# Performance work log

Measured on AMD Instinct MI355X. Metric: run time of the kernel, lower is better.

Reference implementation:

```python
import jax, jax.numpy as jnp
import numpy as np

IN_FEATURES = 16384
OUT_FEATURES = 16384
NNZ = 1_000_000
BATCH = 256


def setup_inputs() -> dict:
    key = jax.random.key(0)
    k_x, k_w, k_b, k_r, k_c = jax.random.split(key, 5)
    x = jax.random.normal(k_x, (BATCH, IN_FEATURES), dtype=jnp.float32)
    weight_vals = jax.random.normal(k_w, (NNZ,), dtype=jnp.float32)
    bias = jax.random.normal(k_b, (OUT_FEATURES,), dtype=jnp.float32)
    rows = jax.random.randint(k_r, (NNZ,), 0, OUT_FEATURES, dtype=jnp.int32)
    cols = jax.random.randint(k_c, (NNZ,), 0, IN_FEATURES, dtype=jnp.int32)
    return {"x": x, "weight_vals": weight_vals, "bias": bias,
            "rows": rows, "cols": cols}


def reference(x, weight_vals, bias, rows, cols):
    # SparseLinear forward: y = x @ W^T + b, with W sparse COO of shape
    # [out_features, in_features]; (rows, cols) are W's nnz coordinates.
    # Per-edge contribution: x[:, col] * W[row, col], scattered into out[:, row].
    contrib = x[:, cols] * weight_vals  # [B, nnz]
    # segment-sum edges into output features: [nnz, B] -> [out, B]
    out = jax.ops.segment_sum(contrib.T, rows, num_segments=OUT_FEATURES).T
    return out + bias  # [B, out_features]
```

## Files before the change

kernel.cpp:

```cpp
#include <hip/hip_runtime.h>
#include <hip/hip_bf16.h>
#include <hip/hip_fp16.h>

#define IN_F    16384
#define OUT_F   16384
#define CAP     128
#define NBUCK   512
#define CAPB    2560
#define EPB     2048
#define TBLK    1024

typedef unsigned int u32x4 __attribute__((ext_vector_type(4)));
typedef float f32x4 __attribute__((ext_vector_type(4)));
typedef float f32x2 __attribute__((ext_vector_type(2)));


__global__ void prep_kernel(const float* __restrict__ x,
                            __hip_bfloat16* __restrict__ xTh,
                            const int* __restrict__ rows,
                            const int* __restrict__ cols,
                            const float* __restrict__ vals, int nnz, int npart,
                            int* __restrict__ gcursor,
                            uint2* __restrict__ staging) {
    __shared__ __align__(16) union {
        float tile[64 * 65];
        struct {
            uint2 recs[EPB];
            int hist[NBUCK];
            int lstart[NBUCK];
            int gbase[NBUCK];
            int wsum[4];
            int total;
        } pa;
    } sm;
    int t = threadIdx.x;
    if ((int)blockIdx.x < npart) {
        sm.pa.hist[t] = 0; sm.pa.hist[t + 256] = 0;
        __syncthreads();
        int i0 = blockIdx.x * EPB;
        unsigned int pk[8], vb[8];
#pragma unroll
        for (int k = 0; k < 8; ++k) {
            int i = i0 + k * 256 + t;
            if (i < nnz) {
                int r = rows[i], c = cols[i];
                pk[k] = ((unsigned int)r << 14) | (unsigned int)c;
                vb[k] = ((unsigned int)c << 16) |
                        (unsigned int)__half_as_ushort(__float2half(vals[i]));
                atomicAdd(&sm.pa.hist[r >> 5], 1);
            } else pk[k] = 0xffffffffu;
        }
        __syncthreads();
        int lane = t & 63, w = t >> 6;
        int h0 = sm.pa.hist[2 * t], h1 = sm.pa.hist[2 * t + 1];
        int pv = h0 + h1;
        int incl = pv;
#pragma unroll
        for (int off = 1; off < 64; off <<= 1) {
            int u = __shfl_up(incl, off, 64);
            if (lane >= off) incl += u;
        }
        if (lane == 63) sm.pa.wsum[w] = incl;
        __syncthreads();
        int addw = 0;
#pragma unroll
        for (int q = 0; q < 3; ++q) addw += (q < w) ? sm.pa.wsum[q] : 0;
        incl += addw;
        int excl = incl - pv;
        sm.pa.lstart[2 * t]     = excl;
        sm.pa.lstart[2 * t + 1] = excl + h0;
        sm.pa.gbase[2 * t]     = h0 > 0 ? atomicAdd(&gcursor[2 * t], h0) : 0;
        sm.pa.gbase[2 * t + 1] = h1 > 0 ? atomicAdd(&gcursor[2 * t + 1], h1) : 0;
        if (t == 255) sm.pa.total = incl;
        sm.pa.hist[t] = 0; sm.pa.hist[t + 256] = 0;
        __syncthreads();
#pragma unroll
        for (int k = 0; k < 8; ++k) {
            if (pk[k] != 0xffffffffu) {
                int b = pk[k] >> 19;
                int pos = sm.pa.lstart[b] + atomicAdd(&sm.pa.hist[b], 1);
                sm.pa.recs[pos] = make_uint2(pk[k], vb[k]);
            }
        }
        __syncthreads();
        int total = sm.pa.total;
        for (int j = t; j < total; j += 256) {
            uint2 rec = sm.pa.recs[j];
            int b = rec.x >> 19;
            int gp = sm.pa.gbase[b] + (j - sm.pa.lstart[b]);
            if (gp < CAPB) {
                unsigned long long pvv =
                    (unsigned long long)rec.x | ((unsigned long long)rec.y << 32);
                __builtin_nontemporal_store(pvv,
                    (unsigned long long*)(staging + (size_t)b * CAPB + gp));
            }
        }
    } else {
        float* tile = (float*)&sm;
        int bid = blockIdx.x - npart;
        int i0 = (bid & 255) * 64;
        int b0 = (bid >> 8) * 64;
        int tx4 = t & 15;
        int r16 = t >> 4;
#pragma unroll
        for (int k = 0; k < 4; ++k) {
            int row = r16 + k * 16;
            f32x4 v = *(const f32x4*)(x + (size_t)(b0 + row) * IN_F + i0 + tx4 * 4);
            tile[row * 65 + tx4 * 4 + 0] = v.x;
            tile[row * 65 + tx4 * 4 + 1] = v.y;
            tile[row * 65 + tx4 * 4 + 2] = v.z;
            tile[row * 65 + tx4 * 4 + 3] = v.w;
        }
        __syncthreads();
        int tx = t & 63, ty = t >> 6;
        int h = b0 >> 7, j0 = b0 & 127;
#pragma unroll
        for (int k = 0; k < 64; k += 4) {
            int col = i0 + ty + k;
            xTh[((size_t)h * IN_F + col) * 128 + j0 + tx] =
                __float2bfloat16(tile[tx * 65 + ty + k]);
        }
    }
}


__global__ void __launch_bounds__(512, 4)
accum_kernel(const unsigned int* __restrict__ xh0,
             const uint2* __restrict__ staging,
             const int* __restrict__ gcursor,
             const float* __restrict__ bias,
             float* __restrict__ out) {
    __shared__ union {
        unsigned int lbin[32 * CAP];
        float slab[32 * 129];
    } u;
    __shared__ int lcnt[32];
    int blk = blockIdx.x;
    int h = blk & 1;
    int bu = blk >> 1;
    int o0 = bu * 32;
    int t = threadIdx.x;
    int w = t >> 6, lane = t & 63;
    {
        u32x4 z = {0u, 0u, 0u, 0u};
#pragma unroll
        for (int i = 0; i < 2; ++i)
            *(u32x4*)&u.lbin[(t + i * 512) * 4] = z;
    }
    if (t < 32) lcnt[t] = 0;
    __syncthreads();
    int n = gcursor[bu];
    if (n > CAPB) n = CAPB;
    const unsigned long long* st =
        (const unsigned long long*)(staging + (size_t)bu * CAPB);
    for (int i = t; i < n; i += 512) {
        unsigned long long v = __builtin_nontemporal_load(st + i);
        unsigned int rx = (unsigned int)v;
        unsigned int ry = (unsigned int)(v >> 32);
        int rl = (rx >> 14) & 31;
        int p = atomicAdd(&lcnt[rl], 1);
        if (p < CAP) u.lbin[rl * CAP + p] = ry;
    }
    __syncthreads();
    const unsigned int* xh = xh0 + (size_t)h * IN_F * 64;
    int rl0 = w * 4;
    int c0 = lcnt[rl0 + 0]; if (c0 > CAP) c0 = CAP;
    int c1 = lcnt[rl0 + 1]; if (c1 > CAP) c1 = CAP;
    int c2 = lcnt[rl0 + 2]; if (c2 > CAP) c2 = CAP;
    int c3 = lcnt[rl0 + 3]; if (c3 > CAP) c3 = CAP;
    int cm01 = c0 > c1 ? c0 : c1;
    int cm23 = c2 > c3 ? c2 : c3;
    int cm = cm01 > cm23 ? cm01 : cm23;
    int lim = (cm + 3) & ~3;
    const u32x4* lb0 = (const u32x4*)&u.lbin[(rl0 + 0) * CAP];
    const u32x4* lb1 = (const u32x4*)&u.lbin[(rl0 + 1) * CAP];
    const u32x4* lb2 = (const u32x4*)&u.lbin[(rl0 + 2) * CAP];
    const u32x4* lb3 = (const u32x4*)&u.lbin[(rl0 + 3) * CAP];
    f32x2 acc[4];
#pragma unroll
    for (int r = 0; r < 4; ++r) acc[r] = (f32x2){0.f, 0.f};
    if (lim > 0) {
        u32x4 cu0 = lb0[0], cu1 = lb1[0], cu2 = lb2[0], cu3 = lb3[0];
        for (int j = 0; j < lim; j += 4) {
            int jn = (j >> 2) + 1;
            u32x4 nx0 = lb0[jn], nx1 = lb1[jn];
            u32x4 nx2 = lb2[jn], nx3 = lb3[jn];
            unsigned int e[16] = {cu0.x, cu0.y, cu0.z, cu0.w,
                                  cu1.x, cu1.y, cu1.z, cu1.w,
                                  cu2.x, cu2.y, cu2.z, cu2.w,
                                  cu3.x, cu3.y, cu3.z, cu3.w};
            unsigned int s[16], g[16];
#pragma unroll
            for (int k = 0; k < 16; ++k) {
                s[k] = __builtin_amdgcn_readfirstlane(e[k]);
                g[k] = *(xh + ((s[k] >> 16) << 6) + lane);
            }
#pragma unroll
            for (int r = 0; r < 4; ++r) {
#pragma unroll
                for (int k = 0; k < 4; ++k) {
                    int q = r * 4 + k;
                    float vv = __half2float(__ushort_as_half(
                                   (unsigned short)(s[q] & 0xffffu)));
                    f32x2 m;
                    m.x = __uint_as_float(g[q] << 16);
                    m.y = __uint_as_float(g[q] & 0xffff0000u);
                    f32x2 v2 = {vv, vv};
                    acc[r] += m * v2;
                }
            }
            cu0 = nx0; cu1 = nx1; cu2 = nx2; cu3 = nx3;
        }
    }
    __syncthreads();
#pragma unroll
    for (int rr = 0; rr < 4; ++rr) {
        int rl = rl0 + rr;
        u.slab[rl * 129 + 2 * lane + 0] = acc[rr].x;
        u.slab[rl * 129 + 2 * lane + 1] = acc[rr].y;
    }
    __syncthreads();
#pragma unroll
    for (int it = 0; it < 2; ++it) {
        int item = t + it * 512;
        int bl = item >> 3;
        int q = item & 7;
        f32x4 bv = *(const f32x4*)(bias + o0 + q * 4);
        f32x4 v;
        v.x = u.slab[(q * 4 + 0) * 129 + bl] + bv.x;
        v.y = u.slab[(q * 4 + 1) * 129 + bl] + bv.y;
        v.z = u.slab[(q * 4 + 2) * 129 + bl] + bv.z;
        v.w = u.slab[(q * 4 + 3) * 129 + bl] + bv.w;
        __builtin_nontemporal_store(v,
            (f32x4*)(out + (size_t)(h * 128 + bl) * OUT_F + o0 + q * 4));
    }
}

extern "C" void kernel_launch(void* const* d_in, const int* in_sizes, int n_in,
                              void* d_out, int out_size, void* d_ws, size_t ws_size,
                              hipStream_t stream) {
    const float* x     = (const float*)d_in[0];
    const float* wvals = (const float*)d_in[1];
    const float* bias  = (const float*)d_in[2];
    const int*   rows  = (const int*)d_in[3];
    const int*   cols  = (const int*)d_in[4];
    float* out = (float*)d_out;
    int nnz = in_sizes[1];

    const size_t MB = 1024 * 1024;
    char* ws = (char*)d_ws;
    __hip_bfloat16* xTh = (__hip_bfloat16*)(ws);
    uint2* staging = (uint2*)(ws + 8 * MB);
    int*   gcursor = (int*)(ws + 20 * MB);

    (void)hipMemsetAsync(gcursor, 0, NBUCK * sizeof(int), stream);

    int npart = (nnz + EPB - 1) / EPB;
    prep_kernel<<<npart + TBLK, 256, 0, stream>>>(x, xTh, rows, cols, wvals, nnz,
                                                  npart, gcursor, staging);
    accum_kernel<<<NBUCK * 2, 512, 0, stream>>>((const unsigned int*)xTh, staging,
                                                gcursor, bias, out);
}
```

Baseline: 146.2 us.

## Process full 256-batch per block instead of splitting batch halves across blocks

Changes the transposed bf16 x layout from two 128-batch halves to a single 256-wide row per input column. Each accum block now covers all 256 batch columns, with each lane loading a uint2 (4 bf16) per edge. The number of blocks is halved, so the staging read and the LDS binning of edges are done once per bucket rather than twice. In exchange there are twice as many accumulators per thread, a larger LDS slab, and fewer blocks to fill the GPU.

```diff
diff --git a/kernel.cpp b/kernel.cpp
--- a/kernel.cpp
+++ b/kernel.cpp
@@ -113,11 +113,10 @@
         }
         __syncthreads();
         int tx = t & 63, ty = t >> 6;
-        int h = b0 >> 7, j0 = b0 & 127;
 #pragma unroll
         for (int k = 0; k < 64; k += 4) {
             int col = i0 + ty + k;
-            xTh[((size_t)h * IN_F + col) * 128 + j0 + tx] =
+            xTh[(size_t)col * 256 + b0 + tx] =
                 __float2bfloat16(tile[tx * 65 + ty + k]);
         }
     }
@@ -125,19 +124,17 @@
 
 
 __global__ void __launch_bounds__(512, 4)
-accum_kernel(const unsigned int* __restrict__ xh0,
+accum_kernel(const uint2* __restrict__ xh2,
              const uint2* __restrict__ staging,
              const int* __restrict__ gcursor,
              const float* __restrict__ bias,
              float* __restrict__ out) {
     __shared__ union {
         unsigned int lbin[32 * CAP];
-        float slab[32 * 129];
+        float slab[32 * 260];
     } u;
     __shared__ int lcnt[32];
-    int blk = blockIdx.x;
-    int h = blk & 1;
-    int bu = blk >> 1;
+    int bu = blockIdx.x;
     int o0 = bu * 32;
     int t = threadIdx.x;
     int w = t >> 6, lane = t & 63;
@@ -162,7 +159,6 @@
         if (p < CAP) u.lbin[rl * CAP + p] = ry;
     }
     __syncthreads();
-    const unsigned int* xh = xh0 + (size_t)h * IN_F * 64;
     int rl0 = w * 4;
     int c0 = lcnt[rl0 + 0]; if (c0 > CAP) c0 = CAP;
     int c1 = lcnt[rl0 + 1]; if (c1 > CAP) c1 = CAP;
@@ -176,9 +172,12 @@
     const u32x4* lb1 = (const u32x4*)&u.lbin[(rl0 + 1) * CAP];
     const u32x4* lb2 = (const u32x4*)&u.lbin[(rl0 + 2) * CAP];
     const u32x4* lb3 = (const u32x4*)&u.lbin[(rl0 + 3) * CAP];
-    f32x2 acc[4];
-#pragma unroll
-    for (int r = 0; r < 4; ++r) acc[r] = (f32x2){0.f, 0.f};
+    f32x2 acc[4][2];
+#pragma unroll
+    for (int r = 0; r < 4; ++r) {
+        acc[r][0] = (f32x2){0.f, 0.f};
+        acc[r][1] = (f32x2){0.f, 0.f};
+    }
     if (lim > 0) {
         u32x4 cu0 = lb0[0], cu1 = lb1[0], cu2 = lb2[0], cu3 = lb3[0];
         for (int j = 0; j < lim; j += 4) {
@@ -189,11 +188,12 @@
                                   cu1.x, cu1.y, cu1.z, cu1.w,
                                   cu2.x, cu2.y, cu2.z, cu2.w,
                                   cu3.x, cu3.y, cu3.z, cu3.w};
-            unsigned int s[16], g[16];
+            unsigned int s[16];
+            uint2 g[16];
 #pragma unroll
             for (int k = 0; k < 16; ++k) {
                 s[k] = __builtin_amdgcn_readfirstlane(e[k]);
-                g[k] = *(xh + ((s[k] >> 16) << 6) + lane);
+                g[k] = xh2[((size_t)(s[k] >> 16) << 6) + lane];
             }
 #pragma unroll
             for (int r = 0; r < 4; ++r) {
@@ -202,11 +202,14 @@
                     int q = r * 4 + k;
                     float vv = __half2float(__ushort_as_half(
                                    (unsigned short)(s[q] & 0xffffu)));
-                    f32x2 m;
-                    m.x = __uint_as_float(g[q] << 16);
-                    m.y = __uint_as_float(g[q] & 0xffff0000u);
                     f32x2 v2 = {vv, vv};
-                    acc[r] += m * v2;
+                    f32x2 m0, m1;
+                    m0.x = __uint_as_float(g[q].x << 16);
+                    m0.y = __uint_as_float(g[q].x & 0xffff0000u);
+                    m1.x = __uint_as_float(g[q].y << 16);
+                    m1.y = __uint_as_float(g[q].y & 0xffff0000u);
+                    acc[r][0] += m0 * v2;
+                    acc[r][1] += m1 * v2;
                 }
             }
             cu0 = nx0; cu1 = nx1; cu2 = nx2; cu3 = nx3;
@@ -216,23 +219,25 @@
 #pragma unroll
     for (int rr = 0; rr < 4; ++rr) {
         int rl = rl0 + rr;
-        u.slab[rl * 129 + 2 * lane + 0] = acc[rr].x;
-        u.slab[rl * 129 + 2 * lane + 1] = acc[rr].y;
-    }
-    __syncthreads();
-#pragma unroll
-    for (int it = 0; it < 2; ++it) {
+        f32x4 v;
+        v.x = acc[rr][0].x; v.y = acc[rr][0].y;
+        v.z = acc[rr][1].x; v.w = acc[rr][1].y;
+        *(f32x4*)&u.slab[rl * 260 + lane * 4] = v;
+    }
+    __syncthreads();
+#pragma unroll
+    for (int it = 0; it < 4; ++it) {
         int item = t + it * 512;
         int bl = item >> 3;
         int q = item & 7;
         f32x4 bv = *(const f32x4*)(bias + o0 + q * 4);
         f32x4 v;
-        v.x = u.slab[(q * 4 + 0) * 129 + bl] + bv.x;
-        v.y = u.slab[(q * 4 + 1) * 129 + bl] + bv.y;
-        v.z = u.slab[(q * 4 + 2) * 129 + bl] + bv.z;
-        v.w = u.slab[(q * 4 + 3) * 129 + bl] + bv.w;
+        v.x = u.slab[(q * 4 + 0) * 260 + bl] + bv.x;
+        v.y = u.slab[(q * 4 + 1) * 260 + bl] + bv.y;
+        v.z = u.slab[(q * 4 + 2) * 260 + bl] + bv.z;
+        v.w = u.slab[(q * 4 + 3) * 260 + bl] + bv.w;
         __builtin_nontemporal_store(v,
-            (f32x4*)(out + (size_t)(h * 128 + bl) * OUT_F + o0 + q * 4));
+            (f32x4*)(out + (size_t)bl * OUT_F + o0 + q * 4));
     }
 }
 
@@ -258,6 +263,6 @@
     int npart = (nnz + EPB - 1) / EPB;
     prep_kernel<<<npart + TBLK, 256, 0, stream>>>(x, xTh, rows, cols, wvals, nnz,
                                                   npart, gcursor, staging);
-    accum_kernel<<<NBUCK * 2, 512, 0, stream>>>((const unsigned int*)xTh, staging,
-                                                gcursor, bias, out);
+    accum_kernel<<<NBUCK, 512, 0, stream>>>((const uint2*)xTh, staging,
+                                            gcursor, bias, out);
 }
```

New measurement: 154.5 us. +5.6%, slower.
